# Kernel optimization log

Measured on AMD Instinct MI355X. Metric: run time of the kernel, lower is better.

## Reference

```python
import jax, jax.numpy as jnp
import numpy as np
import math

NUM_HEADS = 16


def setup_inputs() -> dict:
    key = jax.random.key(0)
    ks = jax.random.split(key, 5)
    L, B, E = 2048, 2, 1024
    scale = 1.0 / math.sqrt(E)
    return {
        "query": jax.random.normal(ks[0], (L, B, E), jnp.float32),
        "key": jax.random.normal(ks[1], (L, B, E), jnp.float32),
        "value": jax.random.normal(ks[2], (L, B, E), jnp.float32),
        "in_proj_weight": jax.random.normal(ks[3], (3 * E, E), jnp.float32) * scale,
        "in_proj_bias": jnp.zeros((3 * E,), jnp.float32),
        "out_w": jax.random.normal(ks[4], (E, E), jnp.float32) * scale,
        "out_b": jnp.zeros((E,), jnp.float32),
    }


def reference(query, key, value, in_proj_weight, in_proj_bias, out_w, out_b):
    L, Bz, E = query.shape
    S = key.shape[0]
    H = NUM_HEADS
    hd = E // H
    # in-projection: chunk packed weight into q/k/v parts (same math as torch chunk)
    w_q, w_k, w_v = jnp.split(in_proj_weight, 3, axis=0)
    b_q, b_k, b_v = jnp.split(in_proj_bias, 3, axis=0)
    q = query @ w_q.T + b_q            # (L, B, E)
    k = key @ w_k.T + b_k              # (S, B, E)
    v = value @ w_v.T + b_v            # (S, B, E)
    # (L, B*H, hd) -> (B*H, L, hd)
    q = q.reshape(L, Bz * H, hd).transpose(1, 0, 2) / math.sqrt(hd)
    k = k.reshape(S, Bz * H, hd).transpose(1, 0, 2)
    v = v.reshape(S, Bz * H, hd).transpose(1, 0, 2)
    # sigmoid attention (non-softmax), full (B*H, L, S) matrix as in original
    attn = jax.nn.sigmoid(jnp.einsum("bld,bsd->bls", q, k))
    denom = attn.sum(axis=-1, keepdims=True) + 1e-4
    out = jnp.einsum("bls,bsd->bld", attn / denom, v)  # (B*H, L, hd)
    out = out.transpose(1, 0, 2).reshape(L, Bz, E)
    out = out @ out_w.T + out_b
    avg_weights = attn.reshape(Bz, H, L, S).sum(axis=1) / H
    return out, avg_weights
```

## Files before the change

kernel.cpp:

```cpp
#include <hip/hip_runtime.h>
#include <stdint.h>


#define L_SEQ 2048
#define NBATCH 2
#define EMB 1024
#define NHEAD 16
#define HD 64
#define MROWS 4096

typedef __bf16 bf16x8 __attribute__((ext_vector_type(8)));
typedef float f32x4 __attribute__((ext_vector_type(4)));

__device__ __forceinline__ unsigned short f2bf(float f) {
  union { float f; uint32_t u; } v; v.f = f;
  uint32_t u = v.u;
  u += 0x7fffu + ((u >> 16) & 1u);
  return (unsigned short)(u >> 16);
}

__device__ __forceinline__ unsigned short f2bf_fast(float f) {
  union { float f; uint32_t u; } v; v.f = f;
  return (unsigned short)((v.u + 0x8000u) >> 16);
}

__device__ __forceinline__ void gl_lds16(const void* gptr, void* ldsptr) {
  const uint32_t* g = reinterpret_cast<const uint32_t*>(gptr);
  auto* l = reinterpret_cast<__attribute__((address_space(3))) uint32_t*>(
      reinterpret_cast<uintptr_t>(ldsptr));
  __builtin_amdgcn_global_load_lds(g, l, 16, 0, 0);
}

__device__ __forceinline__ f32x4 mfma16(bf16x8 a, bf16x8 b, f32x4 c) {
  return __builtin_amdgcn_mfma_f32_16x16x32_bf16(a, b, c, 0, 0, 0);
}

__device__ __forceinline__ float fast_sigmoid(float x) {
  float e = __expf(-x);
  return __builtin_amdgcn_rcpf(1.0f + e);
}

__global__ __launch_bounds__(256) void k_convert(
    const float* __restrict__ qin, const float* __restrict__ kin,
    const float* __restrict__ vin, const float* __restrict__ win,
    const float* __restrict__ wo,
    unsigned short* __restrict__ Xq, unsigned short* __restrict__ Xk,
    unsigned short* __restrict__ Xv, unsigned short* __restrict__ Wb,
    unsigned short* __restrict__ Wob) {
  const int row = blockIdx.x;
  const int t = threadIdx.x;
  const float* src;
  unsigned short* dst;
  int srow;
  size_t drow;
  if (row < 3 * MROWS) {
    const int which = row >> 12;
    const int m = row & (MROWS - 1);
    const int b = m >> 11, l = m & (L_SEQ - 1);
    srow = l * NBATCH + b;
    drow = (size_t)m;
    src = which == 0 ? qin : (which == 1 ? kin : vin);
    dst = which == 0 ? Xq : (which == 1 ? Xk : Xv);
  } else if (row < 3 * MROWS + 3072) {
    srow = row - 3 * MROWS; drow = (size_t)srow; src = win; dst = Wb;
  } else {
    srow = row - (3 * MROWS + 3072); drow = (size_t)srow; src = wo; dst = Wob;
  }
  const float4 vv = *(const float4*)(src + (size_t)srow * EMB + t * 4);
  ushort4 o;
  o.x = f2bf(vv.x); o.y = f2bf(vv.y); o.z = f2bf(vv.z); o.w = f2bf(vv.w);
  *(ushort4*)(dst + drow * EMB + t * 4) = o;
}

__device__ __forceinline__ void gemm_core(
    const unsigned short* __restrict__ A, const unsigned short* __restrict__ Bm,
    int m0, int n0, unsigned short* sA, unsigned short* sB, f32x4 acc[4][4]) {
  const int tid = threadIdx.x;
  const int wave = tid >> 6;
  const int lane = tid & 63;
  const int quad = lane >> 4;
  const int l16 = lane & 15;
  const int wm = (wave >> 1) * 64;
  const int wn = (wave & 1) * 64;
  const int srow = lane >> 2;
  const int scol = lane & 3;

  for (int mi = 0; mi < 4; ++mi)
    for (int ni = 0; ni < 4; ++ni)
      acc[mi][ni] = (f32x4){0.f, 0.f, 0.f, 0.f};

  for (int k0 = 0; k0 < EMB; k0 += 32) {
    __syncthreads();
    for (int i = 0; i < 2; ++i) {
      const int p = wave * 2 + i;
      const int r = p * 16 + srow;
      const int c = scol ^ ((r >> 1) & 3);
      gl_lds16(A + (size_t)(m0 + r) * EMB + k0 + c * 8, sA + p * 512);
      gl_lds16(Bm + (size_t)(n0 + r) * EMB + k0 + c * 8, sB + p * 512);
    }
    __syncthreads();
    bf16x8 af[4], bfr[4];
    for (int mi = 0; mi < 4; ++mi) {
      const int r = wm + mi * 16 + l16;
      const int cp = quad ^ ((r >> 1) & 3);
      af[mi] = *(const bf16x8*)(sA + r * 32 + cp * 8);
    }
    for (int ni = 0; ni < 4; ++ni) {
      const int r = wn + ni * 16 + l16;
      const int cp = quad ^ ((r >> 1) & 3);
      bfr[ni] = *(const bf16x8*)(sB + r * 32 + cp * 8);
    }
    for (int mi = 0; mi < 4; ++mi)
      for (int ni = 0; ni < 4; ++ni)
        acc[mi][ni] = mfma16(af[mi], bfr[ni], acc[mi][ni]);
  }
}

__global__ __launch_bounds__(256) void k_inproj(
    const unsigned short* __restrict__ Xq, const unsigned short* __restrict__ Xk,
    const unsigned short* __restrict__ Xv, const unsigned short* __restrict__ Wb,
    const float* __restrict__ bias,
    unsigned short* __restrict__ qb, unsigned short* __restrict__ kb,
    unsigned short* __restrict__ vb) {
  __shared__ __attribute__((aligned(16))) unsigned short sA[128 * 32];
  __shared__ __attribute__((aligned(16))) unsigned short sB[128 * 32];
  const int z = blockIdx.z;
  const unsigned short* A = z == 0 ? Xq : (z == 1 ? Xk : Xv);
  const int n0 = blockIdx.x * 128, m0 = blockIdx.y * 128;
  f32x4 acc[4][4];
  gemm_core(A, Wb + (size_t)z * EMB * EMB, m0, n0, sA, sB, acc);

  const int tid = threadIdx.x, wave = tid >> 6, lane = tid & 63;
  const int quad = lane >> 4, l16 = lane & 15;
  const int wm = (wave >> 1) * 64, wn = (wave & 1) * 64;
  const float scale = (z == 0) ? 0.125f : 1.0f;
  unsigned short* dst01 = (z == 0) ? qb : kb;
  for (int ni = 0; ni < 4; ++ni) {
    const int n = n0 + wn + ni * 16 + l16;
    const float bv = bias[z * EMB + n];
    const int h = n >> 6, d = n & 63;
    for (int mi = 0; mi < 4; ++mi) {
      for (int r = 0; r < 4; ++r) {
        const int m = m0 + wm + mi * 16 + quad * 4 + r;
        const int b = m >> 11, l = m & (L_SEQ - 1);
        const unsigned short o = f2bf((acc[mi][ni][r] + bv) * scale);
        if (z == 2)
          vb[((size_t)(b * NHEAD + h) * HD + d) * L_SEQ + l] = o;
        else
          dst01[((size_t)(b * NHEAD + h) * L_SEQ + l) * HD + d] = o;
      }
    }
  }
}

__global__ __launch_bounds__(512) void k_attn(
    const unsigned short* __restrict__ qb, const unsigned short* __restrict__ kb,
    const unsigned short* __restrict__ vb, unsigned short* __restrict__ oh) {
  __shared__ __attribute__((aligned(16))) unsigned short sQ[128 * 64];
  __shared__ __attribute__((aligned(16))) unsigned short sK[64 * 64];
  __shared__ __attribute__((aligned(16))) unsigned short sV[64 * 64];
  __shared__ __attribute__((aligned(16))) unsigned short sP[128 * 72];

  const int bh = blockIdx.x;
  const int b = bh >> 4, h = bh & 15;
  const int l0 = blockIdx.y * 128;
  const unsigned short* qg = qb + ((size_t)bh * L_SEQ + l0) * HD;
  const unsigned short* kg = kb + (size_t)bh * L_SEQ * HD;
  const unsigned short* vg = vb + (size_t)bh * HD * L_SEQ;

  const int tid = threadIdx.x, wave = tid >> 6, lane = tid & 63;
  const int quad = lane >> 4, l16 = lane & 15;
  const int sr8 = lane >> 3, sc8 = lane & 7;
  const int sh = (wave >> 2) * 32;
  const int lq = (wave & 3) * 32;

  for (int i = 0; i < 2; ++i) {
    const int p = wave * 2 + i;
    const int r = p * 8 + sr8;
    const int c = sc8 ^ (r & 7);
    gl_lds16(qg + (size_t)r * HD + c * 8, sQ + p * 512);
  }

  f32x4 oacc[4];
  for (int ni = 0; ni < 4; ++ni) oacc[ni] = (f32x4){0.f, 0.f, 0.f, 0.f};
  f32x4 dacc = (f32x4){0.f, 0.f, 0.f, 0.f};

  bf16x8 ones;
  for (int j = 0; j < 8; ++j) ones[j] = (__bf16)1.0f;

  for (int s0 = 0; s0 < L_SEQ; s0 += 64) {
    __syncthreads();
    if (wave < 4) {
      for (int i = 0; i < 2; ++i) {
        const int p = wave * 2 + i;
        const int r = p * 8 + sr8;
        const int c = sc8 ^ (r & 7);
        gl_lds16(kg + (size_t)(s0 + r) * HD + c * 8, sK + p * 512);
      }
    } else {
      for (int i = 0; i < 2; ++i) {
        const int p = (wave - 4) * 2 + i;
        const int r = p * 8 + sr8;
        const int c = sc8 ^ (r & 7);
        gl_lds16(vg + (size_t)r * L_SEQ + s0 + c * 8, sV + p * 512);
      }
    }
    __syncthreads();

    f32x4 st[2][2];
    for (int smi = 0; smi < 2; ++smi)
      for (int lni = 0; lni < 2; ++lni) st[smi][lni] = (f32x4){0.f, 0.f, 0.f, 0.f};
    for (int kk = 0; kk < HD; kk += 32) {
      bf16x8 a[2], bq[2];
      for (int smi = 0; smi < 2; ++smi) {
        const int r = sh + smi * 16 + l16;
        const int c = ((kk >> 3) + quad) ^ (r & 7);
        a[smi] = *(const bf16x8*)(sK + r * 64 + c * 8);
      }
      for (int lni = 0; lni < 2; ++lni) {
        const int r = lq + lni * 16 + l16;
        const int c = ((kk >> 3) + quad) ^ (r & 7);
        bq[lni] = *(const bf16x8*)(sQ + r * 64 + c * 8);
      }
      for (int smi = 0; smi < 2; ++smi)
        for (int lni = 0; lni < 2; ++lni)
          st[smi][lni] = mfma16(a[smi], bq[lni], st[smi][lni]);
    }

    for (int lni = 0; lni < 2; ++lni) {
      const int lrow = lq + lni * 16 + l16;
      for (int smi = 0; smi < 2; ++smi) {
        uint32_t u[4];
        for (int r = 0; r < 4; ++r) {
          union { float f; uint32_t i; } cv;
          cv.f = fast_sigmoid(st[smi][lni][r]);
          u[r] = cv.i + 0x8000u;
        }
        uint2 pk;
        pk.x = __builtin_amdgcn_perm(u[1], u[0], 0x07060302u);
        pk.y = __builtin_amdgcn_perm(u[3], u[2], 0x07060302u);
        *(uint2*)(sP + (size_t)lrow * 72 + sh + smi * 16 + quad * 4) = pk;
      }
    }
    __syncthreads();

    const int lr = wave * 16 + l16;
    for (int kk = 0; kk < 64; kk += 32) {
      bf16x8 ap = *(const bf16x8*)(sP + (size_t)lr * 72 + kk + quad * 8);
      for (int ni = 0; ni < 4; ++ni) {
        const int rd = ni * 16 + l16;
        const int c = ((kk >> 3) + quad) ^ (rd & 7);
        bf16x8 bv4 = *(const bf16x8*)(sV + rd * 64 + c * 8);
        oacc[ni] = mfma16(ap, bv4, oacc[ni]);
      }
      dacc = mfma16(ap, ones, dacc);
    }
  }

  for (int r = 0; r < 4; ++r) {
    const int lrow = l0 + wave * 16 + quad * 4 + r;
    const float rden = __builtin_amdgcn_rcpf(dacc[r] + 1e-4f);
    unsigned short* dst = oh + ((size_t)(b * L_SEQ + lrow)) * EMB + h * HD;
    for (int ni = 0; ni < 4; ++ni)
      dst[ni * 16 + l16] = f2bf_fast(oacc[ni][r] * rden);
  }
}

__global__ __launch_bounds__(512) void k_avg(
    const unsigned short* __restrict__ qb, const unsigned short* __restrict__ kb,
    float* __restrict__ avg) {
  __shared__ __attribute__((aligned(16))) unsigned short sQ[128 * 64];
  __shared__ __attribute__((aligned(16))) unsigned short sK[128 * 64];
  const int ss0 = blockIdx.x * 128, l0 = blockIdx.y * 128, b = blockIdx.z;
  const int tid = threadIdx.x, wave = tid >> 6, lane = tid & 63;
  const int quad = lane >> 4, l16 = lane & 15;
  const int wm = (wave & 1) * 64, wn = (wave >> 1) * 32;
  const int sr8 = lane >> 3, sc8 = lane & 7;

  f32x4 av[4][2];
  for (int mi = 0; mi < 4; ++mi)
    for (int ni = 0; ni < 2; ++ni) av[mi][ni] = (f32x4){0.f, 0.f, 0.f, 0.f};

  for (int h = 0; h < NHEAD; ++h) {
    const unsigned short* qg = qb + ((size_t)(b * NHEAD + h) * L_SEQ + l0) * HD;
    const unsigned short* kg = kb + ((size_t)(b * NHEAD + h) * L_SEQ + ss0) * HD;
    __syncthreads();
    for (int i = 0; i < 2; ++i) {
      const int p = wave * 2 + i;
      const int r = p * 8 + sr8;
      const int c = sc8 ^ (r & 7);
      gl_lds16(qg + (size_t)r * HD + c * 8, sQ + p * 512);
      gl_lds16(kg + (size_t)r * HD + c * 8, sK + p * 512);
    }
    __syncthreads();
    f32x4 scr[4][2];
    for (int mi = 0; mi < 4; ++mi)
      for (int ni = 0; ni < 2; ++ni) scr[mi][ni] = (f32x4){0.f, 0.f, 0.f, 0.f};
    for (int kk = 0; kk < HD; kk += 32) {
      bf16x8 a[4], bb[2];
      for (int mi = 0; mi < 4; ++mi) {
        const int r = wm + mi * 16 + l16;
        const int c = ((kk >> 3) + quad) ^ (r & 7);
        a[mi] = *(const bf16x8*)(sQ + r * 64 + c * 8);
      }
      for (int ni = 0; ni < 2; ++ni) {
        const int r = wn + ni * 16 + l16;
        const int c = ((kk >> 3) + quad) ^ (r & 7);
        bb[ni] = *(const bf16x8*)(sK + r * 64 + c * 8);
      }
      for (int mi = 0; mi < 4; ++mi)
        for (int ni = 0; ni < 2; ++ni)
          scr[mi][ni] = mfma16(a[mi], bb[ni], scr[mi][ni]);
    }
    for (int mi = 0; mi < 4; ++mi)
      for (int ni = 0; ni < 2; ++ni)
        for (int r = 0; r < 4; ++r)
          av[mi][ni][r] += fast_sigmoid(scr[mi][ni][r]);
  }

  for (int mi = 0; mi < 4; ++mi) {
    for (int r = 0; r < 4; ++r) {
      const int l = l0 + wm + mi * 16 + quad * 4 + r;
      float* dst = avg + ((size_t)b * L_SEQ + l) * L_SEQ + ss0 + wn;
      for (int ni = 0; ni < 2; ++ni)
        dst[ni * 16 + l16] = av[mi][ni][r] * 0.0625f;
    }
  }
}

__global__ __launch_bounds__(256) void k_outproj(
    const unsigned short* __restrict__ OH, const unsigned short* __restrict__ Wob,
    const float* __restrict__ ob, float* __restrict__ out) {
  __shared__ __attribute__((aligned(16))) unsigned short sA[128 * 32];
  __shared__ __attribute__((aligned(16))) unsigned short sB[128 * 32];
  const int n0 = blockIdx.x * 128, m0 = blockIdx.y * 128;
  f32x4 acc[4][4];
  gemm_core(OH, Wob, m0, n0, sA, sB, acc);

  const int tid = threadIdx.x, wave = tid >> 6, lane = tid & 63;
  const int quad = lane >> 4, l16 = lane & 15;
  const int wm = (wave >> 1) * 64, wn = (wave & 1) * 64;
  for (int ni = 0; ni < 4; ++ni) {
    const int n = n0 + wn + ni * 16 + l16;
    const float bv = ob[n];
    for (int mi = 0; mi < 4; ++mi) {
      for (int r = 0; r < 4; ++r) {
        const int m = m0 + wm + mi * 16 + quad * 4 + r;
        const int b = m >> 11, l = m & (L_SEQ - 1);
        out[((size_t)l * NBATCH + b) * EMB + n] = acc[mi][ni][r] + bv;
      }
    }
  }
}

extern "C" void kernel_launch(void* const* d_in, const int* in_sizes, int n_in,
                              void* d_out, int out_size, void* d_ws, size_t ws_size,
                              hipStream_t stream) {
  (void)in_sizes; (void)n_in; (void)out_size;
  const float* qin = (const float*)d_in[0];
  const float* kin = (const float*)d_in[1];
  const float* vin = (const float*)d_in[2];
  const float* w   = (const float*)d_in[3];
  const float* bias = (const float*)d_in[4];
  const float* wo  = (const float*)d_in[5];
  const float* ob  = (const float*)d_in[6];
  float* out = (float*)d_out;

  unsigned short* Xq  = (unsigned short*)d_ws;
  unsigned short* Xk  = Xq + (size_t)MROWS * EMB;
  unsigned short* Xv  = Xk + (size_t)MROWS * EMB;
  unsigned short* Wb  = Xv + (size_t)MROWS * EMB;
  unsigned short* Wob = Wb + (size_t)3 * EMB * EMB;
  unsigned short* qbuf = Wob + (size_t)EMB * EMB;
  unsigned short* kbuf = qbuf + (size_t)MROWS * EMB;
  unsigned short* vbuf = kbuf + (size_t)MROWS * EMB;
  unsigned short* ohb  = vbuf + (size_t)MROWS * EMB;
  const size_t need = ((size_t)MROWS * EMB * 7 + (size_t)4 * EMB * EMB) * 2;
  if (ws_size < need) return;

  k_convert<<<16384, 256, 0, stream>>>(qin, kin, vin, w, wo, Xq, Xk, Xv, Wb, Wob);
  k_inproj<<<dim3(8, 32, 3), 256, 0, stream>>>(Xq, Xk, Xv, Wb, bias, qbuf, kbuf, vbuf);
  k_attn<<<dim3(32, 16), 512, 0, stream>>>(qbuf, kbuf, vbuf, ohb);
  k_avg<<<dim3(16, 16, 2), 512, 0, stream>>>(qbuf, kbuf, out + (size_t)MROWS * EMB);
  k_outproj<<<dim3(8, 32), 256, 0, stream>>>(ohb, Wob, ob, out);
}
```

Baseline: 275.7 us.

## Double-buffer attention and avg tiles, use 32x32 MFMA, transpose V via LDS

k_attn and k_avg now double-buffer their K/V and Q/K tiles in LDS. The next tile's global-to-LDS load is issued before the current tile is computed, which removes one barrier per iteration and hides load latency. Both kernels move to 32x32x16 bf16 MFMA, and k_avg grows its tile to 256 key columns. k_inproj stages the V output through a swizzled LDS tile so the transposed writes to vbuf become coalesced 16-byte stores. The cost is much higher LDS use per block (k_avg about 96KB), which may lower occupancy.

```diff
diff --git a/kernel.cpp b/kernel.cpp
--- a/kernel.cpp
+++ b/kernel.cpp
@@ -11,6 +11,7 @@
 
 typedef __bf16 bf16x8 __attribute__((ext_vector_type(8)));
 typedef float f32x4 __attribute__((ext_vector_type(4)));
+typedef float f32x16 __attribute__((ext_vector_type(16)));
 
 __device__ __forceinline__ unsigned short f2bf(float f) {
   union { float f; uint32_t u; } v; v.f = f;
@@ -33,6 +34,10 @@
 
 __device__ __forceinline__ f32x4 mfma16(bf16x8 a, bf16x8 b, f32x4 c) {
   return __builtin_amdgcn_mfma_f32_16x16x32_bf16(a, b, c, 0, 0, 0);
+}
+
+__device__ __forceinline__ f32x16 mfma32(bf16x8 a, bf16x8 b, f32x16 c) {
+  return __builtin_amdgcn_mfma_f32_32x32x16_bf16(a, b, c, 0, 0, 0);
 }
 
 __device__ __forceinline__ float fast_sigmoid(float x) {
@@ -124,6 +129,7 @@
     unsigned short* __restrict__ vb) {
   __shared__ __attribute__((aligned(16))) unsigned short sA[128 * 32];
   __shared__ __attribute__((aligned(16))) unsigned short sB[128 * 32];
+  __shared__ __attribute__((aligned(16))) unsigned short sT[128 * 128];
   const int z = blockIdx.z;
   const unsigned short* A = z == 0 ? Xq : (z == 1 ? Xk : Xv);
   const int n0 = blockIdx.x * 128, m0 = blockIdx.y * 128;
@@ -133,21 +139,51 @@
   const int tid = threadIdx.x, wave = tid >> 6, lane = tid & 63;
   const int quad = lane >> 4, l16 = lane & 15;
   const int wm = (wave >> 1) * 64, wn = (wave & 1) * 64;
-  const float scale = (z == 0) ? 0.125f : 1.0f;
-  unsigned short* dst01 = (z == 0) ? qb : kb;
-  for (int ni = 0; ni < 4; ++ni) {
-    const int n = n0 + wn + ni * 16 + l16;
-    const float bv = bias[z * EMB + n];
-    const int h = n >> 6, d = n & 63;
-    for (int mi = 0; mi < 4; ++mi) {
-      for (int r = 0; r < 4; ++r) {
-        const int m = m0 + wm + mi * 16 + quad * 4 + r;
-        const int b = m >> 11, l = m & (L_SEQ - 1);
-        const unsigned short o = f2bf((acc[mi][ni][r] + bv) * scale);
-        if (z == 2)
-          vb[((size_t)(b * NHEAD + h) * HD + d) * L_SEQ + l] = o;
-        else
-          dst01[((size_t)(b * NHEAD + h) * L_SEQ + l) * HD + d] = o;
+  const int bb = m0 >> 11, lbase = m0 & (L_SEQ - 1);
+
+  if (z == 2) {
+    for (int ni = 0; ni < 4; ++ni) {
+      const int n = wn + ni * 16 + l16;
+      const float bv = bias[2 * EMB + n0 + n];
+      const int x = (n & 15) << 1;
+      for (int mi = 0; mi < 4; ++mi) {
+        const int mchunk = ((wm + mi * 16) >> 2) + quad;
+        const int slot = mchunk ^ x;
+        ushort4 pk;
+        pk.x = f2bf(acc[mi][ni][0] + bv);
+        pk.y = f2bf(acc[mi][ni][1] + bv);
+        pk.z = f2bf(acc[mi][ni][2] + bv);
+        pk.w = f2bf(acc[mi][ni][3] + bv);
+        *(ushort4*)(sT + (size_t)n * 128 + slot * 4) = pk;
+      }
+    }
+    __syncthreads();
+    const int n = tid >> 1, hf = tid & 1;
+    const int ng = n0 + n;
+    const int h = ng >> 6, d = ng & 63;
+    unsigned short* dst =
+        vb + ((size_t)(bb * NHEAD + h) * HD + d) * L_SEQ + lbase + hf * 64;
+    const int x = (n & 15) << 1;
+    for (int j = 0; j < 8; ++j) {
+      const int c2 = hf * 16 + j * 2;
+      const int slot = c2 ^ x;
+      uint4 vd = *(const uint4*)(sT + (size_t)n * 128 + slot * 4);
+      *(uint4*)(dst + j * 8) = vd;
+    }
+  } else {
+    const float scale = (z == 0) ? 0.125f : 1.0f;
+    unsigned short* dst01 = (z == 0) ? qb : kb;
+    for (int ni = 0; ni < 4; ++ni) {
+      const int n = n0 + wn + ni * 16 + l16;
+      const float bv = bias[z * EMB + n];
+      const int h = n >> 6, d = n & 63;
+      for (int mi = 0; mi < 4; ++mi) {
+        for (int r = 0; r < 4; ++r) {
+          const int m = m0 + wm + mi * 16 + quad * 4 + r;
+          const int b = m >> 11, l = m & (L_SEQ - 1);
+          dst01[((size_t)(b * NHEAD + h) * L_SEQ + l) * HD + d] =
+              f2bf((acc[mi][ni][r] + bv) * scale);
+        }
       }
     }
   }
@@ -157,8 +193,8 @@
     const unsigned short* __restrict__ qb, const unsigned short* __restrict__ kb,
     const unsigned short* __restrict__ vb, unsigned short* __restrict__ oh) {
   __shared__ __attribute__((aligned(16))) unsigned short sQ[128 * 64];
-  __shared__ __attribute__((aligned(16))) unsigned short sK[64 * 64];
-  __shared__ __attribute__((aligned(16))) unsigned short sV[64 * 64];
+  __shared__ __attribute__((aligned(16))) unsigned short sK[2][64 * 64];
+  __shared__ __attribute__((aligned(16))) unsigned short sV[2][64 * 64];
   __shared__ __attribute__((aligned(16))) unsigned short sP[128 * 72];
 
   const int bh = blockIdx.x;
@@ -170,9 +206,12 @@
 
   const int tid = threadIdx.x, wave = tid >> 6, lane = tid & 63;
   const int quad = lane >> 4, l16 = lane & 15;
+  const int l32 = lane & 31, lh = lane >> 5;
   const int sr8 = lane >> 3, sc8 = lane & 7;
   const int sh = (wave >> 2) * 32;
   const int lq = (wave & 3) * 32;
+  const int lt = wave & 3;
+  const int dt = wave >> 2;
 
   for (int i = 0; i < 2; ++i) {
     const int p = wave * 2 + i;
@@ -180,32 +219,49 @@
     const int c = sc8 ^ (r & 7);
     gl_lds16(qg + (size_t)r * HD + c * 8, sQ + p * 512);
   }
-
-  f32x4 oacc[4];
-  for (int ni = 0; ni < 4; ++ni) oacc[ni] = (f32x4){0.f, 0.f, 0.f, 0.f};
-  f32x4 dacc = (f32x4){0.f, 0.f, 0.f, 0.f};
-
+  if (wave < 4) {
+    for (int i = 0; i < 2; ++i) {
+      const int p = wave * 2 + i;
+      const int r = p * 8 + sr8;
+      const int c = sc8 ^ (r & 7);
+      gl_lds16(kg + (size_t)r * HD + c * 8, sK[0] + p * 512);
+    }
+  } else {
+    for (int i = 0; i < 2; ++i) {
+      const int p = (wave - 4) * 2 + i;
+      const int r = p * 8 + sr8;
+      const int c = sc8 ^ (r & 7);
+      gl_lds16(vg + (size_t)r * L_SEQ + c * 8, sV[0] + p * 512);
+    }
+  }
+
+  f32x16 oacc, dacc;
+  for (int i = 0; i < 16; ++i) { oacc[i] = 0.f; dacc[i] = 0.f; }
   bf16x8 ones;
   for (int j = 0; j < 8; ++j) ones[j] = (__bf16)1.0f;
 
-  for (int s0 = 0; s0 < L_SEQ; s0 += 64) {
-    __syncthreads();
-    if (wave < 4) {
-      for (int i = 0; i < 2; ++i) {
-        const int p = wave * 2 + i;
-        const int r = p * 8 + sr8;
-        const int c = sc8 ^ (r & 7);
-        gl_lds16(kg + (size_t)(s0 + r) * HD + c * 8, sK + p * 512);
-      }
-    } else {
-      for (int i = 0; i < 2; ++i) {
-        const int p = (wave - 4) * 2 + i;
-        const int r = p * 8 + sr8;
-        const int c = sc8 ^ (r & 7);
-        gl_lds16(vg + (size_t)r * L_SEQ + s0 + c * 8, sV + p * 512);
-      }
-    }
-    __syncthreads();
+  for (int it = 0; it < 32; ++it) {
+    __syncthreads();
+    const int cur = it & 1;
+    if (it < 31) {
+      const int nxt = cur ^ 1;
+      const int s1 = (it + 1) * 64;
+      if (wave < 4) {
+        for (int i = 0; i < 2; ++i) {
+          const int p = wave * 2 + i;
+          const int r = p * 8 + sr8;
+          const int c = sc8 ^ (r & 7);
+          gl_lds16(kg + (size_t)(s1 + r) * HD + c * 8, sK[nxt] + p * 512);
+        }
+      } else {
+        for (int i = 0; i < 2; ++i) {
+          const int p = (wave - 4) * 2 + i;
+          const int r = p * 8 + sr8;
+          const int c = sc8 ^ (r & 7);
+          gl_lds16(vg + (size_t)r * L_SEQ + s1 + c * 8, sV[nxt] + p * 512);
+        }
+      }
+    }
 
     f32x4 st[2][2];
     for (int smi = 0; smi < 2; ++smi)
@@ -215,7 +271,7 @@
       for (int smi = 0; smi < 2; ++smi) {
         const int r = sh + smi * 16 + l16;
         const int c = ((kk >> 3) + quad) ^ (r & 7);
-        a[smi] = *(const bf16x8*)(sK + r * 64 + c * 8);
+        a[smi] = *(const bf16x8*)(sK[cur] + r * 64 + c * 8);
       }
       for (int lni = 0; lni < 2; ++lni) {
         const int r = lq + lni * 16 + l16;
@@ -244,86 +300,104 @@
     }
     __syncthreads();
 
-    const int lr = wave * 16 + l16;
-    for (int kk = 0; kk < 64; kk += 32) {
-      bf16x8 ap = *(const bf16x8*)(sP + (size_t)lr * 72 + kk + quad * 8);
-      for (int ni = 0; ni < 4; ++ni) {
-        const int rd = ni * 16 + l16;
-        const int c = ((kk >> 3) + quad) ^ (rd & 7);
-        bf16x8 bv4 = *(const bf16x8*)(sV + rd * 64 + c * 8);
-        oacc[ni] = mfma16(ap, bv4, oacc[ni]);
-      }
-      dacc = mfma16(ap, ones, dacc);
-    }
-  }
-
-  for (int r = 0; r < 4; ++r) {
-    const int lrow = l0 + wave * 16 + quad * 4 + r;
+    const unsigned short* prow = sP + (size_t)(lt * 32 + l32) * 72;
+    const int vrow = dt * 32 + l32;
+    for (int kk = 0; kk < 4; ++kk) {
+      bf16x8 ap = *(const bf16x8*)(prow + kk * 16 + lh * 8);
+      const int c = (kk * 2 + lh) ^ (vrow & 7);
+      bf16x8 bv = *(const bf16x8*)(sV[cur] + vrow * 64 + c * 8);
+      oacc = mfma32(ap, bv, oacc);
+      dacc = mfma32(ap, ones, dacc);
+    }
+  }
+
+  for (int r = 0; r < 16; ++r) {
+    const int row = (r & 3) + 8 * (r >> 2) + 4 * lh;
+    const int l = l0 + lt * 32 + row;
     const float rden = __builtin_amdgcn_rcpf(dacc[r] + 1e-4f);
-    unsigned short* dst = oh + ((size_t)(b * L_SEQ + lrow)) * EMB + h * HD;
-    for (int ni = 0; ni < 4; ++ni)
-      dst[ni * 16 + l16] = f2bf_fast(oacc[ni][r] * rden);
+    oh[((size_t)(b * L_SEQ + l)) * EMB + h * HD + dt * 32 + l32] =
+        f2bf_fast(oacc[r] * rden);
   }
 }
 
 __global__ __launch_bounds__(512) void k_avg(
     const unsigned short* __restrict__ qb, const unsigned short* __restrict__ kb,
     float* __restrict__ avg) {
-  __shared__ __attribute__((aligned(16))) unsigned short sQ[128 * 64];
-  __shared__ __attribute__((aligned(16))) unsigned short sK[128 * 64];
-  const int ss0 = blockIdx.x * 128, l0 = blockIdx.y * 128, b = blockIdx.z;
+  __shared__ __attribute__((aligned(16))) unsigned short sQ[2][128 * 64];
+  __shared__ __attribute__((aligned(16))) unsigned short sK[2][256 * 64];
+  const int ss0 = blockIdx.x * 256, l0 = blockIdx.y * 128, b = blockIdx.z;
   const int tid = threadIdx.x, wave = tid >> 6, lane = tid & 63;
-  const int quad = lane >> 4, l16 = lane & 15;
-  const int wm = (wave & 1) * 64, wn = (wave >> 1) * 32;
+  const int l32 = lane & 31, lh = lane >> 5;
   const int sr8 = lane >> 3, sc8 = lane & 7;
-
-  f32x4 av[4][2];
-  for (int mi = 0; mi < 4; ++mi)
-    for (int ni = 0; ni < 2; ++ni) av[mi][ni] = (f32x4){0.f, 0.f, 0.f, 0.f};
+  const int mt = wave & 3;
+  const int ntg = (wave >> 2) * 4;
+
+  const unsigned short* qg0 = qb + ((size_t)(b * NHEAD) * L_SEQ + l0) * HD;
+  const unsigned short* kg0 = kb + ((size_t)(b * NHEAD) * L_SEQ + ss0) * HD;
+  const size_t hstride = (size_t)L_SEQ * HD;
+
+  for (int i = 0; i < 2; ++i) {
+    const int p = wave * 2 + i;
+    const int r = p * 8 + sr8;
+    const int c = sc8 ^ (r & 7);
+    gl_lds16(qg0 + (size_t)r * HD + c * 8, sQ[0] + p * 512);
+  }
+  for (int i = 0; i < 4; ++i) {
+    const int p = wave * 4 + i;
+    const int r = p * 8 + sr8;
+    const int c = sc8 ^ (r & 7);
+    gl_lds16(kg0 + (size_t)r * HD + c * 8, sK[0] + p * 512);
+  }
+
+  f32x16 av[4];
+  for (int t = 0; t < 4; ++t)
+    for (int i = 0; i < 16; ++i) av[t][i] = 0.f;
 
   for (int h = 0; h < NHEAD; ++h) {
-    const unsigned short* qg = qb + ((size_t)(b * NHEAD + h) * L_SEQ + l0) * HD;
-    const unsigned short* kg = kb + ((size_t)(b * NHEAD + h) * L_SEQ + ss0) * HD;
-    __syncthreads();
-    for (int i = 0; i < 2; ++i) {
-      const int p = wave * 2 + i;
-      const int r = p * 8 + sr8;
-      const int c = sc8 ^ (r & 7);
-      gl_lds16(qg + (size_t)r * HD + c * 8, sQ + p * 512);
-      gl_lds16(kg + (size_t)r * HD + c * 8, sK + p * 512);
-    }
-    __syncthreads();
-    f32x4 scr[4][2];
-    for (int mi = 0; mi < 4; ++mi)
-      for (int ni = 0; ni < 2; ++ni) scr[mi][ni] = (f32x4){0.f, 0.f, 0.f, 0.f};
-    for (int kk = 0; kk < HD; kk += 32) {
-      bf16x8 a[4], bb[2];
-      for (int mi = 0; mi < 4; ++mi) {
-        const int r = wm + mi * 16 + l16;
-        const int c = ((kk >> 3) + quad) ^ (r & 7);
-        a[mi] = *(const bf16x8*)(sQ + r * 64 + c * 8);
-      }
-      for (int ni = 0; ni < 2; ++ni) {
-        const int r = wn + ni * 16 + l16;
-        const int c = ((kk >> 3) + quad) ^ (r & 7);
-        bb[ni] = *(const bf16x8*)(sK + r * 64 + c * 8);
-      }
-      for (int mi = 0; mi < 4; ++mi)
-        for (int ni = 0; ni < 2; ++ni)
-          scr[mi][ni] = mfma16(a[mi], bb[ni], scr[mi][ni]);
-    }
-    for (int mi = 0; mi < 4; ++mi)
-      for (int ni = 0; ni < 2; ++ni)
-        for (int r = 0; r < 4; ++r)
-          av[mi][ni][r] += fast_sigmoid(scr[mi][ni][r]);
-  }
-
-  for (int mi = 0; mi < 4; ++mi) {
-    for (int r = 0; r < 4; ++r) {
-      const int l = l0 + wm + mi * 16 + quad * 4 + r;
-      float* dst = avg + ((size_t)b * L_SEQ + l) * L_SEQ + ss0 + wn;
-      for (int ni = 0; ni < 2; ++ni)
-        dst[ni * 16 + l16] = av[mi][ni][r] * 0.0625f;
+    __syncthreads();
+    const int cur = h & 1;
+    if (h < NHEAD - 1) {
+      const int nxt = cur ^ 1;
+      const unsigned short* qg = qg0 + (size_t)(h + 1) * hstride;
+      const unsigned short* kg = kg0 + (size_t)(h + 1) * hstride;
+      for (int i = 0; i < 2; ++i) {
+        const int p = wave * 2 + i;
+        const int r = p * 8 + sr8;
+        const int c = sc8 ^ (r & 7);
+        gl_lds16(qg + (size_t)r * HD + c * 8, sQ[nxt] + p * 512);
+      }
+      for (int i = 0; i < 4; ++i) {
+        const int p = wave * 4 + i;
+        const int r = p * 8 + sr8;
+        const int c = sc8 ^ (r & 7);
+        gl_lds16(kg + (size_t)r * HD + c * 8, sK[nxt] + p * 512);
+      }
+    }
+
+    f32x16 scr[4];
+    for (int t = 0; t < 4; ++t)
+      for (int i = 0; i < 16; ++i) scr[t][i] = 0.f;
+    const int qrow = mt * 32 + l32;
+    for (int kk = 0; kk < 4; ++kk) {
+      const int cq = (kk * 2 + lh) ^ (qrow & 7);
+      bf16x8 aq = *(const bf16x8*)(sQ[cur] + qrow * 64 + cq * 8);
+      for (int t = 0; t < 4; ++t) {
+        const int krow = (ntg + t) * 32 + l32;
+        const int ck = (kk * 2 + lh) ^ (krow & 7);
+        bf16x8 bk = *(const bf16x8*)(sK[cur] + krow * 64 + ck * 8);
+        scr[t] = mfma32(aq, bk, scr[t]);
+      }
+    }
+    for (int t = 0; t < 4; ++t)
+      for (int r = 0; r < 16; ++r)
+        av[t][r] += fast_sigmoid(scr[t][r]);
+  }
+
+  for (int t = 0; t < 4; ++t) {
+    for (int r = 0; r < 16; ++r) {
+      const int l = l0 + mt * 32 + (r & 3) + 8 * (r >> 2) + 4 * lh;
+      const int s = ss0 + (ntg + t) * 32 + l32;
+      avg[((size_t)b * L_SEQ + l) * L_SEQ + s] = av[t][r] * 0.0625f;
     }
   }
 }
@@ -381,6 +455,6 @@
   k_convert<<<16384, 256, 0, stream>>>(qin, kin, vin, w, wo, Xq, Xk, Xv, Wb, Wob);
   k_inproj<<<dim3(8, 32, 3), 256, 0, stream>>>(Xq, Xk, Xv, Wb, bias, qbuf, kbuf, vbuf);
   k_attn<<<dim3(32, 16), 512, 0, stream>>>(qbuf, kbuf, vbuf, ohb);
-  k_avg<<<dim3(16, 16, 2), 512, 0, stream>>>(qbuf, kbuf, out + (size_t)MROWS * EMB);
+  k_avg<<<dim3(8, 16, 2), 512, 0, stream>>>(qbuf, kbuf, out + (size_t)MROWS * EMB);
   k_outproj<<<dim3(8, 32), 256, 0, stream>>>(ohb, Wob, ob, out);
 }
```

Result: slower. 290.1 us (+5.2%).
